# Performance work log

Measured on AMD Instinct MI355X. Metric: run time of the kernel, lower is better.

## Reference

```python
import jax, jax.numpy as jnp
import numpy as np

B, L_IN, D_MODEL, CONV_D, KSIZE = 16, 512, 384, 1536, 3
MEL_MAX = 4096
LN_EPS = 1e-5


def _conv1d_same(h, w, b):
    # h: [B, C_in, L], w: [C_out, C_in, K] -> [B, C_out, L]
    y = jax.lax.conv_general_dilated(h, w, window_strides=(1,), padding='SAME',
                                     dimension_numbers=('NCH', 'OIH', 'NCH'))
    return y + b[None, :, None]


def _layernorm(x, g, b):
    m = jnp.mean(x, -1, keepdims=True)
    v = jnp.mean((x - m) ** 2, -1, keepdims=True)
    return (x - m) * jax.lax.rsqrt(v + LN_EPS) * g + b


def _ffn(x, wa, ba, wb, bb):
    # Conv1D_FFT: conv(d_model->conv_d) ReLU conv(conv_d->d_model) ReLU
    h = jnp.transpose(x, (0, 2, 1))
    h = jax.nn.relu(_conv1d_same(h, wa, ba))
    h = jax.nn.relu(_conv1d_same(h, wb, bb))
    return jnp.transpose(h, (0, 2, 1))


def _dur_pred(x, w1, b1, w2, b2, g1, be1, w3, b3, w4, b4, g2, be2, wl, bl):
    h = _ffn(x, w1, b1, w2, b2)
    h = _layernorm(h, g1, be1)  # dropout is identity at eval
    h = _ffn(h, w3, b3, w4, b4)
    h = _layernorm(h, g2, be2)
    return (h @ wl + bl)[..., 0]  # [B, L_in], squeeze(-1)


def _length_regulate(x, dur, mel_max_len):
    # Equivalent to alignment @ x where alignment[b,t,j]=1 iff cum[b,j-1] <= t < cum[b,j],
    # padded with zeros out to mel_max_len (original pads output to mel_max_len).
    cum = jnp.cumsum(dur, axis=-1)                        # [B, L_in]
    total = cum[:, -1]                                    # [B]
    t = jnp.arange(mel_max_len, dtype=cum.dtype)          # [T]
    idx = jax.vmap(lambda c: jnp.searchsorted(c, t, side='right'))(cum)  # [B, T]
    idx = jnp.minimum(idx, x.shape[1] - 1)
    out = jnp.take_along_axis(x, idx[:, :, None], axis=1)  # [B, T, D]
    mask = (t[None, :] < total[:, None])[..., None]
    return out * mask


def setup_inputs() -> dict:
    key = jax.random.key(0)
    ks = jax.random.split(key, 8)
    def nrm(k, shape):
        return jax.random.normal(k, shape, jnp.float32) * 0.02
    return {
        'x': jax.random.normal(ks[0], (B, L_IN, D_MODEL), jnp.float32),
        'target': jax.random.randint(ks[1], (B, L_IN), 0, 8, jnp.int32),
        'mel_max_len': MEL_MAX,
        'w1': nrm(ks[2], (CONV_D, D_MODEL, KSIZE)), 'b1': jnp.zeros((CONV_D,), jnp.float32),
        'w2': nrm(ks[3], (D_MODEL, CONV_D, KSIZE)), 'b2': jnp.zeros((D_MODEL,), jnp.float32),
        'g1': jnp.ones((D_MODEL,), jnp.float32), 'be1': jnp.zeros((D_MODEL,), jnp.float32),
        'w3': nrm(ks[4], (CONV_D, D_MODEL, KSIZE)), 'b3': jnp.zeros((CONV_D,), jnp.float32),
        'w4': nrm(ks[5], (D_MODEL, CONV_D, KSIZE)), 'b4': jnp.zeros((D_MODEL,), jnp.float32),
        'g2': jnp.ones((D_MODEL,), jnp.float32), 'be2': jnp.zeros((D_MODEL,), jnp.float32),
        'wl': nrm(ks[6], (D_MODEL, 1)), 'bl': jnp.zeros((1,), jnp.float32),
    }


def reference(x, target, mel_max_len, w1, b1, w2, b2, g1, be1, w3, b3, w4, b4, g2, be2, wl, bl):
    dur_preds = _dur_pred(x, w1, b1, w2, b2, g1, be1, w3, b3, w4, b4, g2, be2, wl, bl)
    output = _length_regulate(x, target, mel_max_len)
    return (output, dur_preds)
```

## Files before the change

### kernel.cpp

```cpp
#include <hip/hip_runtime.h>
#include <hip/hip_bf16.h>
#include <cstddef>
#include <cstdint>

#define NB 16
#define LIN 512
#define DM 384
#define DC 1536
#define MELMAX 4096
#define LN_EPS 1e-5f

typedef __bf16 bf16x8 __attribute__((ext_vector_type(8)));
typedef float f32x4 __attribute__((ext_vector_type(4)));

#define GL2LDS(gp, lp)                                                                \
    __builtin_amdgcn_global_load_lds((const __attribute__((address_space(1))) void*)(gp), \
                                     (__attribute__((address_space(3))) void*)(lp), 16, 0, 0)

__device__ __forceinline__ float wred(float v) {
#pragma unroll
    for (int m = 32; m >= 1; m >>= 1) v += __shfl_xor(v, m, 64);
    return v;
}

__device__ __forceinline__ unsigned short f2bf(float f) {
    __hip_bfloat16 h = __float2bfloat16(f);
    return *reinterpret_cast<unsigned short*>(&h);
}

__device__ __forceinline__ float bf2f(unsigned short u) {
    return __uint_as_float(((unsigned)u) << 16);
}


__global__ __launch_bounds__(256) void gather_kernel(const float* __restrict__ x,
                                                     const int* __restrict__ cum,
                                                     float* __restrict__ out) {
    const int wid = (blockIdx.x * 256 + threadIdx.x) >> 6;
    const int lane = threadIdx.x & 63;
    const int b = wid >> 12;
    const int t = wid & (MELMAX - 1);
    const int* c = cum + b * LIN;
    const int total = c[LIN - 1];
    float4* orow = reinterpret_cast<float4*>(out + ((size_t)b * MELMAX + t) * DM);
    if (t < total) {
        int lo = 0, hi = LIN;
        while (lo < hi) { int mid = (lo + hi) >> 1; if (c[mid] > t) hi = mid; else lo = mid + 1; }
        const int idx = lo < (LIN - 1) ? lo : (LIN - 1);
        const float4* xrow = reinterpret_cast<const float4*>(x + ((size_t)b * LIN + idx) * DM);
#pragma unroll
        for (int j = 0; j < 2; ++j) {
            const int p = lane + 64 * j;
            if (p < DM / 4) orow[p] = xrow[p];
        }
    } else {
        const float4 z = make_float4(0.f, 0.f, 0.f, 0.f);
#pragma unroll
        for (int j = 0; j < 2; ++j) {
            const int p = lane + 64 * j;
            if (p < DM / 4) orow[p] = z;
        }
    }
}


#define ZPAD_BLKS 96
#define CASTX_BLKS 3072
#define WCAST_BLKS 288
#define PREP_TOTAL (ZPAD_BLKS + CASTX_BLKS + 4 * WCAST_BLKS + NB)

__global__ void prep_kernel(const float* __restrict__ x, unsigned short* __restrict__ xb,
                            unsigned short* __restrict__ hbig, unsigned short* __restrict__ h2b,
                            const float* __restrict__ w1, const float* __restrict__ w2,
                            const float* __restrict__ w3, const float* __restrict__ w4,
                            unsigned short* __restrict__ o1, unsigned short* __restrict__ o2,
                            unsigned short* __restrict__ o3, unsigned short* __restrict__ o4,
                            const int* __restrict__ tgt, int* __restrict__ cum) {
    const int bid = blockIdx.x, tid = threadIdx.x;
    if (bid < ZPAD_BLKS) {
        const int buf = bid >> 5, rem = bid & 31;
        const int b = rem >> 1, row = (rem & 1) ? (LIN + 1) : 0;
        unsigned short* p = buf == 0 ? xb : (buf == 1 ? hbig : h2b);
        const int rl = buf == 1 ? DC : DM;
        unsigned short* base = p + ((size_t)b * (LIN + 2) + row) * rl;
        for (int c = tid; c < rl; c += 256) base[c] = 0;
        return;
    }
    if (bid < ZPAD_BLKS + CASTX_BLKS) {
        const int idx = (bid - ZPAD_BLKS) * 256 + tid;
        const float4 v = reinterpret_cast<const float4*>(x)[idx];
        const int e = idx * 4;
        const int b = e / (LIN * DM);
        const int rem = e - b * (LIN * DM);
        const int l = rem / DM;
        const int c = rem - l * DM;
        ushort4 o;
        o.x = f2bf(v.x); o.y = f2bf(v.y); o.z = f2bf(v.z); o.w = f2bf(v.w);
        *reinterpret_cast<ushort4*>(xb + ((size_t)b * (LIN + 2) + l + 1) * DM + c) = o;
        return;
    }
    if (bid < ZPAD_BLKS + CASTX_BLKS + 4 * WCAST_BLKS) {
        const int j = bid - ZPAD_BLKS - CASTX_BLKS;
        const int which = j / WCAST_BLKS;
        const int idx = (j - which * WCAST_BLKS) * 256 + tid;
        const float* w = which == 0 ? w1 : which == 1 ? w2 : which == 2 ? w3 : w4;
        unsigned short* gg = which == 0 ? o1 : which == 1 ? o2 : which == 2 ? o3 : o4;
        const int CI = (which == 0 || which == 2) ? DM : DC;
        const int OCT = CI / 8;
        const int co = idx / OCT, ci0 = (idx - co * OCT) * 8;
        const float4* p4 = reinterpret_cast<const float4*>(w + (size_t)(co * CI + ci0) * 3);
        float v[24];
#pragma unroll
        for (int q = 0; q < 6; ++q) *reinterpret_cast<float4*>(&v[q * 4]) = p4[q];
        unsigned short tmp[3][8];
#pragma unroll
        for (int e = 0; e < 24; ++e) tmp[e % 3][e / 3] = f2bf(v[e]);
        unsigned short* ob = gg + (size_t)co * (3 * CI) + ci0;
#pragma unroll
        for (int t = 0; t < 3; ++t)
            *reinterpret_cast<uint4*>(ob + (size_t)t * CI) = *reinterpret_cast<const uint4*>(tmp[t]);
        return;
    }
    {
        const int b = bid - (ZPAD_BLKS + CASTX_BLKS + 4 * WCAST_BLKS);
        __shared__ int s[LIN];
        s[tid] = tgt[b * LIN + tid];
        s[tid + 256] = tgt[b * LIN + tid + 256];
        __syncthreads();
        for (int off = 1; off < LIN; off <<= 1) {
            int v0 = (tid >= off) ? s[tid - off] : 0;
            int v1 = (tid + 256 >= off) ? s[tid + 256 - off] : 0;
            __syncthreads();
            s[tid] += v0;
            s[tid + 256] += v1;
            __syncthreads();
        }
        cum[b * LIN + tid] = s[tid];
        cum[b * LIN + tid + 256] = s[tid + 256];
    }
}


__global__ __launch_bounds__(512, 2) void conv8_kernel(const unsigned short* __restrict__ in,
                                                       const unsigned short* __restrict__ wg,
                                                       const float* __restrict__ bias,
                                                       unsigned short* __restrict__ out) {
    constexpr int NKT = 18;
    __shared__ __align__(16) unsigned short smem[65536];

    const int tid = threadIdx.x, lane = tid & 63, wv = tid >> 6;
    const int wrM = wv >> 2, wcN = wv & 3;

    const int orig = blockIdx.x;
    const int wgid = (orig & 7) * 24 + (orig >> 3);
    const int mt = wgid / 6, ng = wgid - mt * 6;
    const int b = mt >> 1, tm = mt & 1;
    const int n0 = ng * 256;

    const unsigned short* inb = in + ((size_t)b * (LIN + 2) + (size_t)tm * 256) * DM;

    const int fr = lane & 15, kg = lane >> 4;

    f32x4 acc[8][4];
#pragma unroll
    for (int i = 0; i < 8; ++i)
#pragma unroll
        for (int j = 0; j < 4; ++j) acc[i][j] = (f32x4){0.f, 0.f, 0.f, 0.f};

#define STG_A(s, H, kt)                                                                   \
    do {                                                                                  \
        const int t_ = (kt) / 6, kc_ = (kt) - t_ * 6;                                     \
        _Pragma("unroll")                                                                 \
        for (int j = 0; j < 2; ++j) {                                                     \
            const int rr = (tid >> 3) + j * 64;                                           \
            const int e = ((tid & 7) * 8) ^ ((rr & 4) << 2);                              \
            GL2LDS(inb + (size_t)(t_ + (H)*128 + rr) * DM + kc_ * 64 + e,                 \
                   smem + (s)*32768 + (H)*8192 + tid * 8 + j * 4096);                     \
        }                                                                                 \
    } while (0)

#define STG_B(s, H, kt)                                                                   \
    do {                                                                                  \
        const int t_ = (kt) / 6, kc_ = (kt) - t_ * 6;                                     \
        _Pragma("unroll")                                                                 \
        for (int j = 0; j < 2; ++j) {                                                     \
            const int rr = (tid >> 3) + j * 64;                                           \
            const int e = ((tid & 7) * 8) ^ ((rr & 4) << 2);                              \
            GL2LDS(wg + (size_t)(n0 + (H)*128 + rr) * 1152 + t_ * 384 + kc_ * 64 + e,     \
                   smem + (s)*32768 + 16384 + (H)*8192 + tid * 8 + j * 4096);             \
        }                                                                                 \
    } while (0)

#define LDA(mh, s)                                                                        \
    do {                                                                                  \
        _Pragma("unroll")                                                                 \
        for (int mf = 0; mf < 4; ++mf)                                                    \
            _Pragma("unroll")                                                             \
            for (int kh = 0; kh < 2; ++kh) {                                              \
                const int rr = (mh)*64 + mf * 16 + fr;                                    \
                const int ke = (kh * 32 + kg * 8) ^ ((rr & 4) << 2);                      \
                aF[mf][kh] = *reinterpret_cast<const bf16x8*>(                            \
                    smem + (s)*32768 + wrM * 8192 + rr * 64 + ke);                        \
            }                                                                             \
    } while (0)

#define LDB(nh, s)                                                                        \
    do {                                                                                  \
        _Pragma("unroll")                                                                 \
        for (int nf = 0; nf < 2; ++nf)                                                    \
            _Pragma("unroll")                                                             \
            for (int kh = 0; kh < 2; ++kh) {                                              \
                const int rr = wcN * 32 + nf * 16 + fr;                                   \
                const int ke = (kh * 32 + kg * 8) ^ ((rr & 4) << 2);                      \
                bF[nf][kh] = *reinterpret_cast<const bf16x8*>(                            \
                    smem + (s)*32768 + 16384 + (nh)*8192 + rr * 64 + ke);                 \
            }                                                                             \
    } while (0)

#define MMA(mh, nh)                                                                       \
    do {                                                                                  \
        _Pragma("unroll")                                                                 \
        for (int mf = 0; mf < 4; ++mf)                                                    \
            _Pragma("unroll")                                                             \
            for (int nf = 0; nf < 2; ++nf)                                                \
                _Pragma("unroll")                                                         \
                for (int kh = 0; kh < 2; ++kh)                                            \
                    acc[(mh)*4 + mf][(nh)*2 + nf] = __builtin_amdgcn_mfma_f32_16x16x32_bf16( \
                        aF[mf][kh], bF[nf][kh], acc[(mh)*4 + mf][(nh)*2 + nf], 0, 0, 0);  \
    } while (0)

    STG_A(0, 0, 0); STG_A(0, 1, 0); STG_B(0, 0, 0); STG_B(0, 1, 0);
    STG_B(1, 0, 1); STG_B(1, 1, 1);
    asm volatile("s_waitcnt vmcnt(4)" ::: "memory");
    asm volatile("s_barrier" ::: "memory");

#pragma unroll 1
    for (int m = 0; m < NKT; ++m) {
        const int s = m & 1, s1 = s ^ 1;
        int k1 = m + 1; if (k1 >= NKT) k1 -= NKT;
        int k2 = m + 2; if (k2 >= NKT) k2 -= NKT;
        bf16x8 aF[4][2], bF[2][2];
        LDA(0, s); LDB(0, s);
        STG_A(s1, 0, k1);
        asm volatile("s_barrier" ::: "memory");
        asm volatile("s_waitcnt lgkmcnt(0)" ::: "memory");
        __builtin_amdgcn_s_setprio(1); MMA(0, 0); __builtin_amdgcn_s_setprio(0);
        asm volatile("s_barrier" ::: "memory");
        LDA(1, s);
        STG_B(s, 0, k2);
        asm volatile("s_barrier" ::: "memory");
        asm volatile("s_waitcnt lgkmcnt(0)" ::: "memory");
        __builtin_amdgcn_s_setprio(1); MMA(1, 0); __builtin_amdgcn_s_setprio(0);
        asm volatile("s_barrier" ::: "memory");
        LDB(1, s);
        STG_A(s1, 1, k1);
        asm volatile("s_barrier" ::: "memory");
        asm volatile("s_waitcnt lgkmcnt(0)" ::: "memory");
        __builtin_amdgcn_s_setprio(1); MMA(1, 1); __builtin_amdgcn_s_setprio(0);
        asm volatile("s_barrier" ::: "memory");
        LDA(0, s);
        STG_B(s, 1, k2);
        asm volatile("s_barrier" ::: "memory");
        asm volatile("s_waitcnt lgkmcnt(0)" ::: "memory");
        __builtin_amdgcn_s_setprio(1); MMA(0, 1); __builtin_amdgcn_s_setprio(0);
        asm volatile("s_waitcnt vmcnt(2)" ::: "memory");
        asm volatile("s_barrier" ::: "memory");
    }
#undef STG_A
#undef STG_B
#undef LDA
#undef LDB
#undef MMA
    asm volatile("s_waitcnt vmcnt(0)" ::: "memory");

    const int fq = lane >> 4;
    float bv[4];
#pragma unroll
    for (int nh = 0; nh < 2; ++nh)
#pragma unroll
        for (int nf = 0; nf < 2; ++nf)
            bv[nh * 2 + nf] = bias[n0 + nh * 128 + wcN * 32 + nf * 16 + fr];
    unsigned short* outb = out + ((size_t)b * (LIN + 2) + (size_t)tm * 256 + 1) * DC;
#pragma unroll
    for (int mh = 0; mh < 2; ++mh)
#pragma unroll
        for (int mf = 0; mf < 4; ++mf)
#pragma unroll
            for (int qy = 0; qy < 4; ++qy) {
                const int r = wrM * 128 + mh * 64 + mf * 16 + fq * 4 + qy;
                unsigned short* orow = outb + (size_t)r * DC + n0;
#pragma unroll
                for (int nh = 0; nh < 2; ++nh)
#pragma unroll
                    for (int nf = 0; nf < 2; ++nf) {
                        const float v = fmaxf(acc[mh * 4 + mf][nh * 2 + nf][qy] + bv[nh * 2 + nf], 0.f);
                        orow[nh * 128 + wcN * 32 + nf * 16 + fr] = f2bf(v);
                    }
            }
}


template <int CI, int CO, int BN>
__global__ __launch_bounds__(256, 2) void conv_mfma_kernel(const unsigned short* __restrict__ in,
                                                           const unsigned short* __restrict__ wg,
                                                           const float* __restrict__ bias,
                                                           unsigned short* __restrict__ out) {
    constexpr int BM = 128, BK = 32;
    constexpr int KC = CI / BK;
    constexpr int AGRP = 12;
    constexpr int GPT = BN / 16;
    constexpr int BGRP = 3 * GPT;
    constexpr int NW_N = BN / 32;
    constexpr int NT = CO / BN;
    constexpr int NCONV = NB * (LIN / BM) * NT;

    __shared__ __align__(16) unsigned short As[2][AGRP * 512];
    __shared__ __align__(16) unsigned short Bs[2][BGRP * 512];

    const int tid = threadIdx.x;
    const int lane = tid & 63;
    const int wv = tid >> 6;

    const int orig = blockIdx.x;
    const int q = NCONV >> 3, xcd = orig & 7, o = orig >> 3;
    const int wgid = xcd * q + o;

    const int mg = wgid / NT;
    const int nt = wgid - mg * NT;
    const int b = mg >> 2;
    const int l0 = (mg & 3) * BM;
    const int n0 = nt * BN;

    const int wr = wv >> 1, wc = wv & 1;

    const unsigned short* inb = in + (size_t)b * (LIN + 2) * CI;

    f32x4 acc[4][NW_N];
#pragma unroll
    for (int m = 0; m < 4; ++m)
#pragma unroll
        for (int n = 0; n < NW_N; ++n) acc[m][n] = (f32x4){0.f, 0.f, 0.f, 0.f};

    const int lrow = lane >> 2;
    const int lch = lane & 3;
    const int fr = lane & 15, kg = lane >> 4;

    const unsigned short* aroot = inb + (size_t)l0 * CI + lch * 8;
    const unsigned short* broot = wg + (size_t)n0 * (3 * CI) + lch * 8;

#define STAGE(c, kb)                                                                      \
    do {                                                                                  \
        const unsigned short* abase = aroot + (kb) * BK;                                  \
        _Pragma("unroll")                                                                 \
        for (int g = wv; g < AGRP; g += 4) {                                              \
            const int sg = g < 9 ? g : 0;                                                 \
            GL2LDS(abase + (size_t)(sg * 16 + lrow) * CI, &As[c][g * 512]);               \
        }                                                                                 \
        const unsigned short* bbase = broot + (kb) * BK;                                  \
        _Pragma("unroll")                                                                 \
        for (int g2 = wv; g2 < BGRP; g2 += 4) {                                           \
            const int t = g2 / GPT, gr = g2 - t * GPT;                                    \
            GL2LDS(bbase + (size_t)(gr * 16 + lrow) * (3 * CI) + (size_t)t * CI,          \
                   &Bs[c][g2 * 512]);                                                     \
        }                                                                                 \
    } while (0)

#define COMPUTE(c)                                                                        \
    do {                                                                                  \
        _Pragma("unroll")                                                                 \
        for (int t = 0; t < 3; ++t) {                                                     \
            bf16x8 aF[4], bF[NW_N];                                                       \
            _Pragma("unroll")                                                             \
            for (int m = 0; m < 4; ++m)                                                   \
                aF[m] = *reinterpret_cast<const bf16x8*>(                                 \
                    &As[c][(t + wr * 64 + m * 16 + fr) * BK + kg * 8]);                   \
            _Pragma("unroll")                                                             \
            for (int n = 0; n < NW_N; ++n)                                                \
                bF[n] = *reinterpret_cast<const bf16x8*>(                                 \
                    &Bs[c][(t * BN + wc * (BN / 2) + n * 16 + fr) * BK + kg * 8]);        \
            _Pragma("unroll")                                                             \
            for (int m = 0; m < 4; ++m)                                                   \
                _Pragma("unroll")                                                         \
                for (int n = 0; n < NW_N; ++n)                                            \
                    acc[m][n] =                                                           \
                        __builtin_amdgcn_mfma_f32_16x16x32_bf16(aF[m], bF[n], acc[m][n],  \
                                                                0, 0, 0);                 \
        }                                                                                 \
    } while (0)

    STAGE(0, 0);
    STAGE(1, 1);
#pragma unroll 1
    for (int kb = 0; kb < KC; ++kb) {
        const int cur = kb & 1;
        if constexpr (BN == 128)
            asm volatile("s_waitcnt vmcnt(9)" ::: "memory");
        else
            asm volatile("s_waitcnt vmcnt(6)" ::: "memory");
        __builtin_amdgcn_sched_barrier(0);
        __builtin_amdgcn_s_barrier();
        __builtin_amdgcn_sched_barrier(0);
        COMPUTE(cur);
        asm volatile("s_waitcnt lgkmcnt(0)" ::: "memory");
        __builtin_amdgcn_sched_barrier(0);
        __builtin_amdgcn_s_barrier();
        __builtin_amdgcn_sched_barrier(0);
        int nk = kb + 2;
        if (nk >= KC) nk -= KC;
        STAGE(cur, nk);
    }
#undef STAGE
#undef COMPUTE
    asm volatile("s_waitcnt vmcnt(0)" ::: "memory");

    const int fq = lane >> 4;
    float bv[NW_N];
#pragma unroll
    for (int n = 0; n < NW_N; ++n) bv[n] = bias[n0 + wc * (BN / 2) + n * 16 + fr];
    unsigned short* outb = out + (size_t)b * (LIN + 2) * CO;
#pragma unroll
    for (int m = 0; m < 4; ++m)
#pragma unroll
        for (int qy = 0; qy < 4; ++qy) {
            const int grow = l0 + wr * 64 + m * 16 + fq * 4 + qy + 1;
            unsigned short* orow = outb + (size_t)grow * CO + n0 + wc * (BN / 2) + fr;
#pragma unroll
            for (int n = 0; n < NW_N; ++n) {
                const float v = fmaxf(acc[m][n][qy] + bv[n], 0.f);
                orow[n * 16] = f2bf(v);
            }
        }
}


__global__ __launch_bounds__(256) void ln_kernel(unsigned short* __restrict__ h,
                                                 const float* __restrict__ g,
                                                 const float* __restrict__ be) {
    const int row = blockIdx.x * 4 + (threadIdx.x >> 6);
    const int lane = threadIdx.x & 63;
    const int b = row >> 9, l = row & (LIN - 1);
    unsigned short* hr = h + ((size_t)b * (LIN + 2) + l + 1) * DM;
    float v[6];
    float s = 0.f;
#pragma unroll
    for (int j = 0; j < 6; ++j) { v[j] = bf2f(hr[lane + 64 * j]); s += v[j]; }
    s = wred(s);
    const float mean = s * (1.f / DM);
    float vs = 0.f;
#pragma unroll
    for (int j = 0; j < 6; ++j) { const float d = v[j] - mean; vs += d * d; }
    vs = wred(vs);
    const float rstd = rsqrtf(vs * (1.f / DM) + LN_EPS);
#pragma unroll
    for (int j = 0; j < 6; ++j) {
        const int c = lane + 64 * j;
        hr[c] = f2bf((v[j] - mean) * rstd * g[c] + be[c]);
    }
}


__global__ __launch_bounds__(256) void ln_linear_kernel(const unsigned short* __restrict__ h,
                                                        const float* __restrict__ g,
                                                        const float* __restrict__ be,
                                                        const float* __restrict__ wl,
                                                        const float* __restrict__ bl,
                                                        float* __restrict__ dur) {
    const int row = blockIdx.x * 4 + (threadIdx.x >> 6);
    const int lane = threadIdx.x & 63;
    const int b = row >> 9, l = row & (LIN - 1);
    const unsigned short* hr = h + ((size_t)b * (LIN + 2) + l + 1) * DM;
    float v[6];
    float s = 0.f;
#pragma unroll
    for (int j = 0; j < 6; ++j) { v[j] = bf2f(hr[lane + 64 * j]); s += v[j]; }
    s = wred(s);
    const float mean = s * (1.f / DM);
    float vs = 0.f;
#pragma unroll
    for (int j = 0; j < 6; ++j) { const float d = v[j] - mean; vs += d * d; }
    vs = wred(vs);
    const float rstd = rsqrtf(vs * (1.f / DM) + LN_EPS);
    float dot = 0.f;
#pragma unroll
    for (int j = 0; j < 6; ++j) {
        const int c = lane + 64 * j;
        dot += ((v[j] - mean) * rstd * g[c] + be[c]) * wl[c];
    }
    dot = wred(dot);
    if (lane == 0) dur[row] = dot + bl[0];
}


extern "C" void kernel_launch(void* const* d_in, const int* in_sizes, int n_in,
                              void* d_out, int out_size, void* d_ws, size_t ws_size,
                              hipStream_t stream) {
    const float* x   = (const float*)d_in[0];
    const int*   tgt = (const int*)d_in[1];
    const float* w1  = (const float*)d_in[3];
    const float* b1  = (const float*)d_in[4];
    const float* w2  = (const float*)d_in[5];
    const float* b2  = (const float*)d_in[6];
    const float* g1  = (const float*)d_in[7];
    const float* be1 = (const float*)d_in[8];
    const float* w3  = (const float*)d_in[9];
    const float* b3  = (const float*)d_in[10];
    const float* w4  = (const float*)d_in[11];
    const float* b4  = (const float*)d_in[12];
    const float* g2  = (const float*)d_in[13];
    const float* be2 = (const float*)d_in[14];
    const float* wl  = (const float*)d_in[15];
    const float* bl  = (const float*)d_in[16];

    float* out = (float*)d_out;
    float* dur = out + (size_t)NB * MELMAX * DM;

    unsigned short* ws = (unsigned short*)d_ws;
    unsigned short* xb   = ws;
    unsigned short* hbig = xb + (size_t)NB * (LIN + 2) * DM;
    unsigned short* h2b  = hbig + (size_t)NB * (LIN + 2) * DC;
    unsigned short* wg1  = h2b + (size_t)NB * (LIN + 2) * DM;
    unsigned short* wg2  = wg1 + (size_t)DC * 3 * DM;
    unsigned short* wg3  = wg2 + (size_t)DM * 3 * DC;
    unsigned short* wg4  = wg3 + (size_t)DC * 3 * DM;
    int* cum = (int*)(wg4 + (size_t)DM * 3 * DC);

    prep_kernel<<<PREP_TOTAL, 256, 0, stream>>>(x, xb, hbig, h2b, w1, w2, w3, w4,
                                                wg1, wg2, wg3, wg4, tgt, cum);

    gather_kernel<<<(NB * MELMAX) / 4, 256, 0, stream>>>(x, cum, out);

    conv8_kernel<<<NB * 2 * (DC / 256), 512, 0, stream>>>(xb, wg1, b1, hbig);
    conv_mfma_kernel<DC, DM, 64><<<NB * (LIN / 128) * (DM / 64), 256, 0, stream>>>(hbig, wg2, b2, h2b);
    ln_kernel<<<NB * LIN / 4, 256, 0, stream>>>(h2b, g1, be1);
    conv8_kernel<<<NB * 2 * (DC / 256), 512, 0, stream>>>(h2b, wg3, b3, hbig);
    conv_mfma_kernel<DC, DM, 64><<<NB * (LIN / 128) * (DM / 64), 256, 0, stream>>>(hbig, wg4, b4, xb);
    ln_linear_kernel<<<NB * LIN / 4, 256, 0, stream>>>(xb, g2, be2, wl, bl, dur);
}
```

Measured before the change: 216.8 us.

## Retile first FFN conv to 128x384 tiles over exactly 256 workgroups

The d_model->conv_d conv kernel switches from 256x256 output tiles (192 workgroups) to 128x384 tiles (256 workgroups). Each wave now computes a 64x96 slice with six N-chunks, and the staging and MFMA schedule is rebuilt into three phases per K step. The aim is to fill all 256 compute units on MI355X in a single wave of workgroups, removing the partial second wave or idle units. The cost is lower arithmetic intensity per tile, with more A and B reloads per output, and a new barrier and waitcnt schedule that must stay correct.

```diff
diff --git a/kernel.cpp b/kernel.cpp
--- a/kernel.cpp
+++ b/kernel.cpp
@@ -141,7 +141,7 @@
 }
 
 
-__global__ __launch_bounds__(512, 2) void conv8_kernel(const unsigned short* __restrict__ in,
+__global__ __launch_bounds__(512, 2) void conv6_kernel(const unsigned short* __restrict__ in,
                                                        const unsigned short* __restrict__ wg,
                                                        const float* __restrict__ bias,
                                                        unsigned short* __restrict__ out) {
@@ -152,86 +152,82 @@
     const int wrM = wv >> 2, wcN = wv & 3;
 
     const int orig = blockIdx.x;
-    const int wgid = (orig & 7) * 24 + (orig >> 3);
-    const int mt = wgid / 6, ng = wgid - mt * 6;
-    const int b = mt >> 1, tm = mt & 1;
-    const int n0 = ng * 256;
-
-    const unsigned short* inb = in + ((size_t)b * (LIN + 2) + (size_t)tm * 256) * DM;
+    const int wgid = (orig & 7) * 32 + (orig >> 3);
+    const int mg = wgid >> 2, ng = wgid & 3;
+    const int b = mg >> 2, tm = mg & 3;
+    const int n0 = ng * 384;
+
+    const unsigned short* inb = in + ((size_t)b * (LIN + 2) + (size_t)tm * 128) * DM;
 
     const int fr = lane & 15, kg = lane >> 4;
 
-    f32x4 acc[8][4];
-#pragma unroll
-    for (int i = 0; i < 8; ++i)
-#pragma unroll
-        for (int j = 0; j < 4; ++j) acc[i][j] = (f32x4){0.f, 0.f, 0.f, 0.f};
-
-#define STG_A(s, H, kt)                                                                   \
+    f32x4 acc[4][6];
+#pragma unroll
+    for (int i = 0; i < 4; ++i)
+#pragma unroll
+        for (int j = 0; j < 6; ++j) acc[i][j] = (f32x4){0.f, 0.f, 0.f, 0.f};
+
+#define STG_A6(s, kt)                                                                     \
     do {                                                                                  \
         const int t_ = (kt) / 6, kc_ = (kt) - t_ * 6;                                     \
         _Pragma("unroll")                                                                 \
         for (int j = 0; j < 2; ++j) {                                                     \
             const int rr = (tid >> 3) + j * 64;                                           \
             const int e = ((tid & 7) * 8) ^ ((rr & 4) << 2);                              \
-            GL2LDS(inb + (size_t)(t_ + (H)*128 + rr) * DM + kc_ * 64 + e,                 \
-                   smem + (s)*32768 + (H)*8192 + tid * 8 + j * 4096);                     \
+            GL2LDS(inb + (size_t)(t_ + rr) * DM + kc_ * 64 + e,                           \
+                   smem + (s)*32768 + j * 4096 + tid * 8);                                \
         }                                                                                 \
     } while (0)
 
-#define STG_B(s, H, kt)                                                                   \
+#define STG_B6(s, c, kt)                                                                  \
     do {                                                                                  \
         const int t_ = (kt) / 6, kc_ = (kt) - t_ * 6;                                     \
-        _Pragma("unroll")                                                                 \
-        for (int j = 0; j < 2; ++j) {                                                     \
-            const int rr = (tid >> 3) + j * 64;                                           \
-            const int e = ((tid & 7) * 8) ^ ((rr & 4) << 2);                              \
-            GL2LDS(wg + (size_t)(n0 + (H)*128 + rr) * 1152 + t_ * 384 + kc_ * 64 + e,     \
-                   smem + (s)*32768 + 16384 + (H)*8192 + tid * 8 + j * 4096);             \
-        }                                                                                 \
-    } while (0)
-
-#define LDA(mh, s)                                                                        \
+        const int rr = tid >> 3;                                                          \
+        const int e = ((tid & 7) * 8) ^ ((rr & 4) << 2);                                  \
+        GL2LDS(wg + (size_t)(n0 + (c)*64 + rr) * 1152 + t_ * 384 + kc_ * 64 + e,          \
+               smem + (s)*32768 + 8192 + (c)*4096 + tid * 8);                             \
+    } while (0)
+
+#define LDA6(s)                                                                           \
     do {                                                                                  \
         _Pragma("unroll")                                                                 \
         for (int mf = 0; mf < 4; ++mf)                                                    \
             _Pragma("unroll")                                                             \
             for (int kh = 0; kh < 2; ++kh) {                                              \
-                const int rr = (mh)*64 + mf * 16 + fr;                                    \
+                const int rr = wrM * 64 + mf * 16 + fr;                                   \
                 const int ke = (kh * 32 + kg * 8) ^ ((rr & 4) << 2);                      \
                 aF[mf][kh] = *reinterpret_cast<const bf16x8*>(                            \
-                    smem + (s)*32768 + wrM * 8192 + rr * 64 + ke);                        \
+                    smem + (s)*32768 + rr * 64 + ke);                                     \
             }                                                                             \
     } while (0)
 
-#define LDB(nh, s)                                                                        \
-    do {                                                                                  \
-        _Pragma("unroll")                                                                 \
-        for (int nf = 0; nf < 2; ++nf)                                                    \
-            _Pragma("unroll")                                                             \
-            for (int kh = 0; kh < 2; ++kh) {                                              \
-                const int rr = wcN * 32 + nf * 16 + fr;                                   \
-                const int ke = (kh * 32 + kg * 8) ^ ((rr & 4) << 2);                      \
-                bF[nf][kh] = *reinterpret_cast<const bf16x8*>(                            \
-                    smem + (s)*32768 + 16384 + (nh)*8192 + rr * 64 + ke);                 \
-            }                                                                             \
-    } while (0)
-
-#define MMA(mh, nh)                                                                       \
+#define LDB6(c, idx, s)                                                                   \
+    do {                                                                                  \
+        _Pragma("unroll")                                                                 \
+        for (int kh = 0; kh < 2; ++kh) {                                                  \
+            const int rr = wcN * 16 + fr;                                                 \
+            const int ke = (kh * 32 + kg * 8) ^ ((rr & 4) << 2);                          \
+            bF[idx][kh] = *reinterpret_cast<const bf16x8*>(                               \
+                smem + (s)*32768 + 8192 + (c)*4096 + rr * 64 + ke);                       \
+        }                                                                                 \
+    } while (0)
+
+#define MMA6(c, idx)                                                                      \
     do {                                                                                  \
         _Pragma("unroll")                                                                 \
         for (int mf = 0; mf < 4; ++mf)                                                    \
             _Pragma("unroll")                                                             \
-            for (int nf = 0; nf < 2; ++nf)                                                \
-                _Pragma("unroll")                                                         \
-                for (int kh = 0; kh < 2; ++kh)                                            \
-                    acc[(mh)*4 + mf][(nh)*2 + nf] = __builtin_amdgcn_mfma_f32_16x16x32_bf16( \
-                        aF[mf][kh], bF[nf][kh], acc[(mh)*4 + mf][(nh)*2 + nf], 0, 0, 0);  \
-    } while (0)
-
-    STG_A(0, 0, 0); STG_A(0, 1, 0); STG_B(0, 0, 0); STG_B(0, 1, 0);
-    STG_B(1, 0, 1); STG_B(1, 1, 1);
-    asm volatile("s_waitcnt vmcnt(4)" ::: "memory");
+            for (int kh = 0; kh < 2; ++kh)                                                \
+                acc[mf][c] = __builtin_amdgcn_mfma_f32_16x16x32_bf16(                     \
+                    aF[mf][kh], bF[idx][kh], acc[mf][c], 0, 0, 0);                        \
+    } while (0)
+
+    STG_A6(0, 0);
+#pragma unroll
+    for (int c = 0; c < 6; ++c) STG_B6(0, c, 0);
+#pragma unroll
+    for (int c = 0; c < 6; ++c) STG_B6(1, c, 1);
+    asm volatile("s_waitcnt vmcnt(6)" ::: "memory");
     asm volatile("s_barrier" ::: "memory");
 
 #pragma unroll 1
@@ -240,63 +236,52 @@
         int k1 = m + 1; if (k1 >= NKT) k1 -= NKT;
         int k2 = m + 2; if (k2 >= NKT) k2 -= NKT;
         bf16x8 aF[4][2], bF[2][2];
-        LDA(0, s); LDB(0, s);
-        STG_A(s1, 0, k1);
+        LDA6(s); LDB6(0, 0, s); LDB6(1, 1, s);
+        STG_A6(s1, k1);
         asm volatile("s_barrier" ::: "memory");
         asm volatile("s_waitcnt lgkmcnt(0)" ::: "memory");
-        __builtin_amdgcn_s_setprio(1); MMA(0, 0); __builtin_amdgcn_s_setprio(0);
-        asm volatile("s_barrier" ::: "memory");
-        LDA(1, s);
-        STG_B(s, 0, k2);
+        __builtin_amdgcn_s_setprio(1); MMA6(0, 0); MMA6(1, 1); __builtin_amdgcn_s_setprio(0);
+        asm volatile("s_barrier" ::: "memory");
+        LDB6(2, 0, s); LDB6(3, 1, s);
+        STG_B6(s, 0, k2); STG_B6(s, 1, k2);
         asm volatile("s_barrier" ::: "memory");
         asm volatile("s_waitcnt lgkmcnt(0)" ::: "memory");
-        __builtin_amdgcn_s_setprio(1); MMA(1, 0); __builtin_amdgcn_s_setprio(0);
-        asm volatile("s_barrier" ::: "memory");
-        LDB(1, s);
-        STG_A(s1, 1, k1);
+        __builtin_amdgcn_s_setprio(1); MMA6(2, 0); MMA6(3, 1); __builtin_amdgcn_s_setprio(0);
+        asm volatile("s_barrier" ::: "memory");
+        LDB6(4, 0, s); LDB6(5, 1, s);
+        STG_B6(s, 2, k2); STG_B6(s, 3, k2);
         asm volatile("s_barrier" ::: "memory");
         asm volatile("s_waitcnt lgkmcnt(0)" ::: "memory");
-        __builtin_amdgcn_s_setprio(1); MMA(1, 1); __builtin_amdgcn_s_setprio(0);
-        asm volatile("s_barrier" ::: "memory");
-        LDA(0, s);
-        STG_B(s, 1, k2);
-        asm volatile("s_barrier" ::: "memory");
-        asm volatile("s_waitcnt lgkmcnt(0)" ::: "memory");
-        __builtin_amdgcn_s_setprio(1); MMA(0, 1); __builtin_amdgcn_s_setprio(0);
-        asm volatile("s_waitcnt vmcnt(2)" ::: "memory");
-        asm volatile("s_barrier" ::: "memory");
-    }
-#undef STG_A
-#undef STG_B
-#undef LDA
-#undef LDB
-#undef MMA
+        __builtin_amdgcn_s_setprio(1); MMA6(4, 0); MMA6(5, 1); __builtin_amdgcn_s_setprio(0);
+        asm volatile("s_barrier" ::: "memory");
+        STG_B6(s, 4, k2); STG_B6(s, 5, k2);
+        asm volatile("s_waitcnt vmcnt(6)" ::: "memory");
+        asm volatile("s_barrier" ::: "memory");
+    }
+#undef STG_A6
+#undef STG_B6
+#undef LDA6
+#undef LDB6
+#undef MMA6
     asm volatile("s_waitcnt vmcnt(0)" ::: "memory");
 
     const int fq = lane >> 4;
-    float bv[4];
-#pragma unroll
-    for (int nh = 0; nh < 2; ++nh)
-#pragma unroll
-        for (int nf = 0; nf < 2; ++nf)
-            bv[nh * 2 + nf] = bias[n0 + nh * 128 + wcN * 32 + nf * 16 + fr];
-    unsigned short* outb = out + ((size_t)b * (LIN + 2) + (size_t)tm * 256 + 1) * DC;
-#pragma unroll
-    for (int mh = 0; mh < 2; ++mh)
-#pragma unroll
-        for (int mf = 0; mf < 4; ++mf)
-#pragma unroll
-            for (int qy = 0; qy < 4; ++qy) {
-                const int r = wrM * 128 + mh * 64 + mf * 16 + fq * 4 + qy;
-                unsigned short* orow = outb + (size_t)r * DC + n0;
-#pragma unroll
-                for (int nh = 0; nh < 2; ++nh)
-#pragma unroll
-                    for (int nf = 0; nf < 2; ++nf) {
-                        const float v = fmaxf(acc[mh * 4 + mf][nh * 2 + nf][qy] + bv[nh * 2 + nf], 0.f);
-                        orow[nh * 128 + wcN * 32 + nf * 16 + fr] = f2bf(v);
-                    }
+    float bv[6];
+#pragma unroll
+    for (int c = 0; c < 6; ++c) bv[c] = bias[n0 + c * 64 + wcN * 16 + fr];
+    unsigned short* outb = out + ((size_t)b * (LIN + 2) + (size_t)tm * 128 + 1) * DC;
+#pragma unroll
+    for (int mf = 0; mf < 4; ++mf)
+#pragma unroll
+        for (int qy = 0; qy < 4; ++qy) {
+            const int r = wrM * 64 + mf * 16 + fq * 4 + qy;
+            unsigned short* orow = outb + (size_t)r * DC + n0 + wcN * 16 + fr;
+#pragma unroll
+            for (int c = 0; c < 6; ++c) {
+                const float v = fmaxf(acc[mf][c][qy] + bv[c], 0.f);
+                orow[c * 64] = f2bf(v);
             }
+        }
 }
 
 
@@ -529,10 +514,10 @@
 
     gather_kernel<<<(NB * MELMAX) / 4, 256, 0, stream>>>(x, cum, out);
 
-    conv8_kernel<<<NB * 2 * (DC / 256), 512, 0, stream>>>(xb, wg1, b1, hbig);
+    conv6_kernel<<<256, 512, 0, stream>>>(xb, wg1, b1, hbig);
     conv_mfma_kernel<DC, DM, 64><<<NB * (LIN / 128) * (DM / 64), 256, 0, stream>>>(hbig, wg2, b2, h2b);
     ln_kernel<<<NB * LIN / 4, 256, 0, stream>>>(h2b, g1, be1);
-    conv8_kernel<<<NB * 2 * (DC / 256), 512, 0, stream>>>(h2b, wg3, b3, hbig);
+    conv6_kernel<<<256, 512, 0, stream>>>(h2b, wg3, b3, hbig);
     conv_mfma_kernel<DC, DM, 64><<<NB * (LIN / 128) * (DM / 64), 256, 0, stream>>>(hbig, wg4, b4, xb);
     ln_linear_kernel<<<NB * LIN / 4, 256, 0, stream>>>(xb, g2, be2, wl, bl, dur);
 }
```

Result: faster. 203.9 us (-5.9%).
